# Kernel tuning notes

Measured on AMD Instinct MI355X. Metric: run time of the kernel, lower is better.

The kernel has to match this reference:

```python
import jax, jax.numpy as jnp
import numpy as np

B = 262144
INPUT_DIM = 512
HID = 64
NUM_BASE = 2
NUM_CLASSES = 2


def setup_inputs() -> dict:
    key = jax.random.key(0)
    ks = jax.random.split(key, 10)
    probs = jax.random.uniform(ks[0], (B, NUM_BASE, NUM_CLASSES), dtype=jnp.float32)
    fuzzy_features = jax.random.normal(ks[1], (B, INPUT_DIM), dtype=jnp.float32)
    s1 = 1.0 / np.sqrt(INPUT_DIM)
    s2 = 1.0 / np.sqrt(HID)
    # m1: Linear(input_dim,64) -> ReLU -> Linear(64, num_base*num_classes)
    W1 = jax.random.uniform(ks[2], (INPUT_DIM, HID), jnp.float32, -s1, s1)
    b1 = jax.random.uniform(ks[3], (HID,), jnp.float32, -s1, s1)
    W2 = jax.random.uniform(ks[4], (HID, NUM_BASE * NUM_CLASSES), jnp.float32, -s2, s2)
    b2 = jax.random.uniform(ks[5], (NUM_BASE * NUM_CLASSES,), jnp.float32, -s2, s2)
    # m2: Linear(input_dim,64) -> ReLU -> Linear(64, num_classes)
    W3 = jax.random.uniform(ks[6], (INPUT_DIM, HID), jnp.float32, -s1, s1)
    b3 = jax.random.uniform(ks[7], (HID,), jnp.float32, -s1, s1)
    W4 = jax.random.uniform(ks[8], (HID, NUM_CLASSES), jnp.float32, -s2, s2)
    b4 = jax.random.uniform(ks[9], (NUM_CLASSES,), jnp.float32, -s2, s2)
    return {"probs": probs, "fuzzy_features": fuzzy_features,
            "W1": W1, "b1": b1, "W2": W2, "b2": b2,
            "W3": W3, "b3": b3, "W4": W4, "b4": b4}


def _forward(probs, x, W1, b1, W2, b2, W3, b3, W4, b4):
    # FuzzyMeasureLearner
    h1 = jax.nn.relu(x @ W1 + b1)                       # [B, 64]
    single = jax.nn.sigmoid((h1 @ W2 + b2).reshape(-1, NUM_BASE, NUM_CLASSES))
    h2 = jax.nn.relu(x @ W3 + b3)                       # [B, 64]
    inc = jax.nn.sigmoid(h2 @ W4 + b4)                  # [B, 2]
    # Vectorized Choquet integral (binary, 2 sources)
    p0 = probs[:, 0, :]                                 # [B, 2]
    p1 = probs[:, 1, :]
    mu1 = single[:, 0, :]
    mu2 = single[:, 1, :]
    mu12 = jnp.minimum(jnp.maximum(mu1, mu2) + inc, 1.0)
    res = jnp.where(p0 <= p1,
                    p0 * mu1 + (p1 - p0) * mu12,
                    p1 * mu2 + (p0 - p1) * mu12)        # [B, 2]
    return jax.nn.softmax(res, axis=1)


def reference(probs, fuzzy_features, W1, b1, W2, b2, W3, b3, W4, b4):
    return _forward(probs, fuzzy_features, W1, b1, W2, b2, W3, b3, W4, b4)
```

## Files before the change

### kernel.cpp

```cpp
#include <hip/hip_runtime.h>

typedef short s16x8 __attribute__((ext_vector_type(8)));
typedef float f32x4 __attribute__((ext_vector_type(4)));
typedef float f32x2 __attribute__((ext_vector_type(2)));

static __device__ __forceinline__ short f2bf(float f) {
    unsigned u = __builtin_bit_cast(unsigned, f);
    unsigned r = (u + 0x7fffu + ((u >> 16) & 1u)) >> 16;
    return (short)r;
}

__global__ void prep_weights(const float* __restrict__ W1,
                             const float* __restrict__ W3,
                             short* __restrict__ bws) {
    int tid = blockIdx.x * blockDim.x + threadIdx.x;
    int j  = tid & 7;
    int l  = (tid >> 3) & 63;
    int nt = (tid >> 9) & 7;
    int kk = tid >> 12;
    int k = kk * 32 + ((l >> 4) << 3) + j;
    int n = nt * 16 + (l & 15);
    float v = (n < 64) ? W1[k * 64 + n] : W3[k * 64 + (n - 64)];
    bws[tid] = f2bf(v);
}

__global__ __launch_bounds__(256, 2)
void mf2_main(const float* __restrict__ probs, const float* __restrict__ x,
              const short* __restrict__ bws,
              const float* __restrict__ b1, const float* __restrict__ W2,
              const float* __restrict__ b2, const float* __restrict__ b3,
              const float* __restrict__ W4, const float* __restrict__ b4,
              float* __restrict__ out)
{
    const int lane = threadIdx.x & 63;
    const int wv   = threadIdx.x >> 6;
    const int g    = lane >> 4;
    const int m    = lane & 15;
    const long rowBase = (long)blockIdx.x * 128 + wv * 32;

    float w2r[4][4];
    float w4r[4][2];
    float biasr[8];
    #pragma unroll
    for (int nt = 0; nt < 4; ++nt) {
        const int col = m + 16 * nt;
        #pragma unroll
        for (int c = 0; c < 4; ++c) w2r[nt][c] = W2[col * 4 + c];
        #pragma unroll
        for (int c = 0; c < 2; ++c) w4r[nt][c] = W4[col * 2 + c];
    }
    #pragma unroll
    for (int nt = 0; nt < 8; ++nt) {
        const int col = m + 16 * nt;
        biasr[nt] = (col < 64) ? b1[col] : b3[col - 64];
    }
    float b2v[4], b4v[2];
    #pragma unroll
    for (int c = 0; c < 4; ++c) b2v[c] = b2[c];
    #pragma unroll
    for (int c = 0; c < 2; ++c) b4v[c] = b4[c];

    f32x4 acc[2][8];
    #pragma unroll
    for (int t = 0; t < 2; ++t)
        #pragma unroll
        for (int nt = 0; nt < 8; ++nt)
            acc[t][nt] = (f32x4){0.f, 0.f, 0.f, 0.f};

    const float* xp = x + (rowBase + m) * 512 + g * 8;

    #pragma unroll 2
    for (int kk = 0; kk < 16; ++kk) {
        s16x8 a[2];
        #pragma unroll
        for (int t = 0; t < 2; ++t) {
            const float* p = xp + t * (16 * 512) + kk * 32;
            f32x4 lo = *(const f32x4*)p;
            f32x4 hi = *(const f32x4*)(p + 4);
            s16x8 av;
            av[0] = f2bf(lo[0]); av[1] = f2bf(lo[1]);
            av[2] = f2bf(lo[2]); av[3] = f2bf(lo[3]);
            av[4] = f2bf(hi[0]); av[5] = f2bf(hi[1]);
            av[6] = f2bf(hi[2]); av[7] = f2bf(hi[3]);
            a[t] = av;
        }
        const s16x8* bp = (const s16x8*)(bws + kk * 4096) + lane;
        #pragma unroll
        for (int nt = 0; nt < 8; ++nt) {
            s16x8 b = bp[nt * 64];
            acc[0][nt] = __builtin_amdgcn_mfma_f32_16x16x32_bf16(a[0], b, acc[0][nt], 0, 0, 0);
            acc[1][nt] = __builtin_amdgcn_mfma_f32_16x16x32_bf16(a[1], b, acc[1][nt], 0, 0, 0);
        }
    }

    float own[6] = {0.f, 0.f, 0.f, 0.f, 0.f, 0.f};
    #pragma unroll
    for (int t = 0; t < 2; ++t) {
        #pragma unroll
        for (int r = 0; r < 4; ++r) {
            float v[6] = {0.f, 0.f, 0.f, 0.f, 0.f, 0.f};
            #pragma unroll
            for (int nt = 0; nt < 4; ++nt) {
                float h = fmaxf(acc[t][nt][r] + biasr[nt], 0.f);
                v[0] += h * w2r[nt][0];
                v[1] += h * w2r[nt][1];
                v[2] += h * w2r[nt][2];
                v[3] += h * w2r[nt][3];
            }
            #pragma unroll
            for (int j = 0; j < 4; ++j) {
                float h = fmaxf(acc[t][4 + j][r] + biasr[4 + j], 0.f);
                v[4] += h * w4r[j][0];
                v[5] += h * w4r[j][1];
            }
            #pragma unroll
            for (int msk = 1; msk <= 8; msk <<= 1) {
                #pragma unroll
                for (int c = 0; c < 6; ++c) v[c] += __shfl_xor(v[c], msk, 64);
            }
            if (m == t * 4 + r) {
                #pragma unroll
                for (int c = 0; c < 6; ++c) own[c] = v[c];
            }
        }
    }

    if (m < 8) {
        const int t = m >> 2, r = m & 3;
        const long row = rowBase + t * 16 + g * 4 + r;
        f32x4 pr = *(const f32x4*)(probs + row * 4);
        float mu1[2], mu2[2], icv[2];
        #pragma unroll
        for (int c = 0; c < 2; ++c) {
            mu1[c] = 1.0f / (1.0f + __expf(-(own[c]     + b2v[c])));
            mu2[c] = 1.0f / (1.0f + __expf(-(own[2 + c] + b2v[2 + c])));
            icv[c] = 1.0f / (1.0f + __expf(-(own[4 + c] + b4v[c])));
        }
        float res[2];
        #pragma unroll
        for (int c = 0; c < 2; ++c) {
            float p0 = pr[c], p1 = pr[2 + c];
            float m12 = fminf(fmaxf(mu1[c], mu2[c]) + icv[c], 1.0f);
            res[c] = (p0 <= p1) ? (p0 * mu1[c] + (p1 - p0) * m12)
                                : (p1 * mu2[c] + (p0 - p1) * m12);
        }
        float d01 = res[0] - res[1];
        f32x2 o;
        o[0] = 1.0f / (1.0f + __expf(-d01));
        o[1] = 1.0f / (1.0f + __expf(d01));
        *(f32x2*)(out + row * 2) = o;
    }
}

extern "C" void kernel_launch(void* const* d_in, const int* in_sizes, int n_in,
                              void* d_out, int out_size, void* d_ws, size_t ws_size,
                              hipStream_t stream)
{
    const float* probs = (const float*)d_in[0];
    const float* x     = (const float*)d_in[1];
    const float* W1    = (const float*)d_in[2];
    const float* b1    = (const float*)d_in[3];
    const float* W2    = (const float*)d_in[4];
    const float* b2    = (const float*)d_in[5];
    const float* W3    = (const float*)d_in[6];
    const float* b3    = (const float*)d_in[7];
    const float* W4    = (const float*)d_in[8];
    const float* b4    = (const float*)d_in[9];
    float* out = (float*)d_out;
    short* bws = (short*)d_ws;

    hipLaunchKernelGGL(prep_weights, dim3(256), dim3(256), 0, stream, W1, W3, bws);
    hipLaunchKernelGGL(mf2_main, dim3(2048), dim3(256), 0, stream,
                       probs, x, bws, b1, W2, b2, b3, W4, b4, out);
}
```

Before: 143.4 us.

## Double rows per wave, prefetch x one K-step ahead, packed bf16 convert

Each wave now handles 64 rows instead of 32, so each B-weight fragment load is reused across four M tiles, and the grid is halved. The x loads for the next K step are issued before the MFMAs of the current step, as nontemporal loads, to overlap global latency with compute. Float-to-bf16 conversion uses the packed intrinsic instead of manual rounding, and the W2/W4 loads are vectorised. Accumulator registers double (128 VGPRs of accumulators), which may strain the 2-waves-per-SIMD launch bound and cause spills or lower occupancy.

```diff
diff --git a/kernel.cpp b/kernel.cpp
--- a/kernel.cpp
+++ b/kernel.cpp
@@ -1,6 +1,8 @@
 #include <hip/hip_runtime.h>
+#include <hip/hip_bf16.h>
 
 typedef short s16x8 __attribute__((ext_vector_type(8)));
+typedef unsigned u32x4 __attribute__((ext_vector_type(4)));
 typedef float f32x4 __attribute__((ext_vector_type(4)));
 typedef float f32x2 __attribute__((ext_vector_type(2)));
 
@@ -8,6 +10,13 @@
     unsigned u = __builtin_bit_cast(unsigned, f);
     unsigned r = (u + 0x7fffu + ((u >> 16) & 1u)) >> 16;
     return (short)r;
+}
+
+static __device__ __forceinline__ unsigned pk2bf(float a, float b) {
+    __hip_bfloat162 h = __float22bfloat162_rn(make_float2(a, b));
+    unsigned r;
+    __builtin_memcpy(&r, &h, sizeof(r));
+    return r;
 }
 
 __global__ void prep_weights(const float* __restrict__ W1,
@@ -36,7 +45,58 @@
     const int wv   = threadIdx.x >> 6;
     const int g    = lane >> 4;
     const int m    = lane & 15;
-    const long rowBase = (long)blockIdx.x * 128 + wv * 32;
+    const long rowBase = (long)blockIdx.x * 256 + wv * 64;
+
+    f32x4 acc[4][8];
+    #pragma unroll
+    for (int t = 0; t < 4; ++t)
+        #pragma unroll
+        for (int nt = 0; nt < 8; ++nt)
+            acc[t][nt] = (f32x4){0.f, 0.f, 0.f, 0.f};
+
+    const float* xp = x + (rowBase + m) * 512 + g * 8;
+    const s16x8* bp = (const s16x8*)bws + lane;
+
+    f32x4 ra[4][2];
+    #pragma unroll
+    for (int t = 0; t < 4; ++t) {
+        const float* p = xp + t * (16 * 512);
+        ra[t][0] = __builtin_nontemporal_load((const f32x4*)p);
+        ra[t][1] = __builtin_nontemporal_load((const f32x4*)(p + 4));
+    }
+
+    #pragma unroll 2
+    for (int kk = 0; kk < 16; ++kk) {
+        s16x8 b[8];
+        #pragma unroll
+        for (int nt = 0; nt < 8; ++nt) b[nt] = bp[kk * 512 + nt * 64];
+
+        s16x8 a[4];
+        #pragma unroll
+        for (int t = 0; t < 4; ++t) {
+            u32x4 pa;
+            pa[0] = pk2bf(ra[t][0][0], ra[t][0][1]);
+            pa[1] = pk2bf(ra[t][0][2], ra[t][0][3]);
+            pa[2] = pk2bf(ra[t][1][0], ra[t][1][1]);
+            pa[3] = pk2bf(ra[t][1][2], ra[t][1][3]);
+            a[t] = __builtin_bit_cast(s16x8, pa);
+        }
+
+        if (kk < 15) {
+            #pragma unroll
+            for (int t = 0; t < 4; ++t) {
+                const float* p = xp + t * (16 * 512) + (kk + 1) * 32;
+                ra[t][0] = __builtin_nontemporal_load((const f32x4*)p);
+                ra[t][1] = __builtin_nontemporal_load((const f32x4*)(p + 4));
+            }
+        }
+
+        #pragma unroll
+        for (int nt = 0; nt < 8; ++nt)
+            #pragma unroll
+            for (int t = 0; t < 4; ++t)
+                acc[t][nt] = __builtin_amdgcn_mfma_f32_16x16x32_bf16(a[t], b[nt], acc[t][nt], 0, 0, 0);
+    }
 
     float w2r[4][4];
     float w4r[4][2];
@@ -44,10 +104,11 @@
     #pragma unroll
     for (int nt = 0; nt < 4; ++nt) {
         const int col = m + 16 * nt;
-        #pragma unroll
-        for (int c = 0; c < 4; ++c) w2r[nt][c] = W2[col * 4 + c];
-        #pragma unroll
-        for (int c = 0; c < 2; ++c) w4r[nt][c] = W4[col * 2 + c];
+        f32x4 w2v = *(const f32x4*)(W2 + col * 4);
+        #pragma unroll
+        for (int c = 0; c < 4; ++c) w2r[nt][c] = w2v[c];
+        f32x2 w4v = *(const f32x2*)(W4 + col * 2);
+        w4r[nt][0] = w4v[0]; w4r[nt][1] = w4v[1];
     }
     #pragma unroll
     for (int nt = 0; nt < 8; ++nt) {
@@ -60,42 +121,9 @@
     #pragma unroll
     for (int c = 0; c < 2; ++c) b4v[c] = b4[c];
 
-    f32x4 acc[2][8];
-    #pragma unroll
-    for (int t = 0; t < 2; ++t)
-        #pragma unroll
-        for (int nt = 0; nt < 8; ++nt)
-            acc[t][nt] = (f32x4){0.f, 0.f, 0.f, 0.f};
-
-    const float* xp = x + (rowBase + m) * 512 + g * 8;
-
-    #pragma unroll 2
-    for (int kk = 0; kk < 16; ++kk) {
-        s16x8 a[2];
-        #pragma unroll
-        for (int t = 0; t < 2; ++t) {
-            const float* p = xp + t * (16 * 512) + kk * 32;
-            f32x4 lo = *(const f32x4*)p;
-            f32x4 hi = *(const f32x4*)(p + 4);
-            s16x8 av;
-            av[0] = f2bf(lo[0]); av[1] = f2bf(lo[1]);
-            av[2] = f2bf(lo[2]); av[3] = f2bf(lo[3]);
-            av[4] = f2bf(hi[0]); av[5] = f2bf(hi[1]);
-            av[6] = f2bf(hi[2]); av[7] = f2bf(hi[3]);
-            a[t] = av;
-        }
-        const s16x8* bp = (const s16x8*)(bws + kk * 4096) + lane;
-        #pragma unroll
-        for (int nt = 0; nt < 8; ++nt) {
-            s16x8 b = bp[nt * 64];
-            acc[0][nt] = __builtin_amdgcn_mfma_f32_16x16x32_bf16(a[0], b, acc[0][nt], 0, 0, 0);
-            acc[1][nt] = __builtin_amdgcn_mfma_f32_16x16x32_bf16(a[1], b, acc[1][nt], 0, 0, 0);
-        }
-    }
-
     float own[6] = {0.f, 0.f, 0.f, 0.f, 0.f, 0.f};
     #pragma unroll
-    for (int t = 0; t < 2; ++t) {
+    for (int t = 0; t < 4; ++t) {
         #pragma unroll
         for (int r = 0; r < 4; ++r) {
             float v[6] = {0.f, 0.f, 0.f, 0.f, 0.f, 0.f};
@@ -125,7 +153,7 @@
         }
     }
 
-    if (m < 8) {
+    {
         const int t = m >> 2, r = m & 3;
         const long row = rowBase + t * 16 + g * 4 + r;
         f32x4 pr = *(const f32x4*)(probs + row * 4);
@@ -170,6 +198,6 @@
     short* bws = (short*)d_ws;
 
     hipLaunchKernelGGL(prep_weights, dim3(256), dim3(256), 0, stream, W1, W3, bws);
-    hipLaunchKernelGGL(mf2_main, dim3(2048), dim3(256), 0, stream,
+    hipLaunchKernelGGL(mf2_main, dim3(1024), dim3(256), 0, stream,
                        probs, x, bws, b1, W2, b2, b3, W4, b4, out);
 }
```

New measurement: 146.4 us. +2.1%, slower.

## Stage bf16 weights in LDS with 1024-thread blocks and packed bf16 conversion

Applied to the files above, without the earlier changes.

Each block now copies the whole 128 KB pre-packed bf16 weight matrix into shared memory and reads B fragments from LDS instead of global memory. Blocks grow to 1024 threads covering 512 rows, and the grid shrinks to 512. The fp32-to-bf16 conversion of x switches to the packed two-element HIP intrinsic, and loads of the epilogue weights and biases move after the MFMA loop to lower register pressure during it. The cost is a 128 KB LDS footprint per block, which likely limits occupancy to one block per CU, and a copy-in phase plus barrier before any compute.

```diff
diff --git a/kernel.cpp b/kernel.cpp
--- a/kernel.cpp
+++ b/kernel.cpp
@@ -1,6 +1,8 @@
 #include <hip/hip_runtime.h>
+#include <hip/hip_bf16.h>
 
 typedef short s16x8 __attribute__((ext_vector_type(8)));
+typedef unsigned u32x4 __attribute__((ext_vector_type(4)));
 typedef float f32x4 __attribute__((ext_vector_type(4)));
 typedef float f32x2 __attribute__((ext_vector_type(2)));
 
@@ -8,6 +10,13 @@
     unsigned u = __builtin_bit_cast(unsigned, f);
     unsigned r = (u + 0x7fffu + ((u >> 16) & 1u)) >> 16;
     return (short)r;
+}
+
+static __device__ __forceinline__ unsigned pk2bf(float a, float b) {
+    __hip_bfloat162 h = __float22bfloat162_rn(make_float2(a, b));
+    unsigned r;
+    __builtin_memcpy(&r, &h, sizeof(r));
+    return r;
 }
 
 __global__ void prep_weights(const float* __restrict__ W1,
@@ -24,7 +33,7 @@
     bws[tid] = f2bf(v);
 }
 
-__global__ __launch_bounds__(256, 2)
+__global__ __launch_bounds__(1024, 4)
 void mf2_main(const float* __restrict__ probs, const float* __restrict__ x,
               const short* __restrict__ bws,
               const float* __restrict__ b1, const float* __restrict__ W2,
@@ -32,11 +41,58 @@
               const float* __restrict__ W4, const float* __restrict__ b4,
               float* __restrict__ out)
 {
-    const int lane = threadIdx.x & 63;
-    const int wv   = threadIdx.x >> 6;
+    __shared__ short bsh[512 * 128];
+
+    const int tid  = threadIdx.x;
+    const int lane = tid & 63;
+    const int wv   = tid >> 6;
     const int g    = lane >> 4;
     const int m    = lane & 15;
-    const long rowBase = (long)blockIdx.x * 128 + wv * 32;
+    const long rowBase = (long)blockIdx.x * 512 + wv * 32;
+
+    {
+        const f32x4* src = (const f32x4*)bws;
+        f32x4* dst = (f32x4*)bsh;
+        #pragma unroll
+        for (int it = 0; it < 8; ++it) {
+            const int idx = it * 1024 + tid;
+            dst[idx] = src[idx];
+        }
+    }
+    __syncthreads();
+
+    f32x4 acc[2][8];
+    #pragma unroll
+    for (int t = 0; t < 2; ++t)
+        #pragma unroll
+        for (int nt = 0; nt < 8; ++nt)
+            acc[t][nt] = (f32x4){0.f, 0.f, 0.f, 0.f};
+
+    const float* xp = x + (rowBase + m) * 512 + g * 8;
+    const s16x8* bls = (const s16x8*)bsh + lane;
+
+    #pragma unroll 2
+    for (int kk = 0; kk < 16; ++kk) {
+        s16x8 a[2];
+        #pragma unroll
+        for (int t = 0; t < 2; ++t) {
+            const float* p = xp + t * (16 * 512) + kk * 32;
+            f32x4 lo = *(const f32x4*)p;
+            f32x4 hi = *(const f32x4*)(p + 4);
+            u32x4 pa;
+            pa[0] = pk2bf(lo[0], lo[1]);
+            pa[1] = pk2bf(lo[2], lo[3]);
+            pa[2] = pk2bf(hi[0], hi[1]);
+            pa[3] = pk2bf(hi[2], hi[3]);
+            a[t] = __builtin_bit_cast(s16x8, pa);
+        }
+        #pragma unroll
+        for (int nt = 0; nt < 8; ++nt) {
+            s16x8 b = bls[kk * 512 + nt * 64];
+            acc[0][nt] = __builtin_amdgcn_mfma_f32_16x16x32_bf16(a[0], b, acc[0][nt], 0, 0, 0);
+            acc[1][nt] = __builtin_amdgcn_mfma_f32_16x16x32_bf16(a[1], b, acc[1][nt], 0, 0, 0);
+        }
+    }
 
     float w2r[4][4];
     float w4r[4][2];
@@ -44,10 +100,11 @@
     #pragma unroll
     for (int nt = 0; nt < 4; ++nt) {
         const int col = m + 16 * nt;
+        f32x4 w2v = *(const f32x4*)(W2 + col * 4);
         #pragma unroll
-        for (int c = 0; c < 4; ++c) w2r[nt][c] = W2[col * 4 + c];
-        #pragma unroll
-        for (int c = 0; c < 2; ++c) w4r[nt][c] = W4[col * 2 + c];
+        for (int c = 0; c < 4; ++c) w2r[nt][c] = w2v[c];
+        f32x2 w4v = *(const f32x2*)(W4 + col * 2);
+        w4r[nt][0] = w4v[0]; w4r[nt][1] = w4v[1];
     }
     #pragma unroll
     for (int nt = 0; nt < 8; ++nt) {
@@ -59,39 +116,6 @@
     for (int c = 0; c < 4; ++c) b2v[c] = b2[c];
     #pragma unroll
     for (int c = 0; c < 2; ++c) b4v[c] = b4[c];
-
-    f32x4 acc[2][8];
-    #pragma unroll
-    for (int t = 0; t < 2; ++t)
-        #pragma unroll
-        for (int nt = 0; nt < 8; ++nt)
-            acc[t][nt] = (f32x4){0.f, 0.f, 0.f, 0.f};
-
-    const float* xp = x + (rowBase + m) * 512 + g * 8;
-
-    #pragma unroll 2
-    for (int kk = 0; kk < 16; ++kk) {
-        s16x8 a[2];
-        #pragma unroll
-        for (int t = 0; t < 2; ++t) {
-            const float* p = xp + t * (16 * 512) + kk * 32;
-            f32x4 lo = *(const f32x4*)p;
-            f32x4 hi = *(const f32x4*)(p + 4);
-            s16x8 av;
-            av[0] = f2bf(lo[0]); av[1] = f2bf(lo[1]);
-            av[2] = f2bf(lo[2]); av[3] = f2bf(lo[3]);
-            av[4] = f2bf(hi[0]); av[5] = f2bf(hi[1]);
-            av[6] = f2bf(hi[2]); av[7] = f2bf(hi[3]);
-            a[t] = av;
-        }
-        const s16x8* bp = (const s16x8*)(bws + kk * 4096) + lane;
-        #pragma unroll
-        for (int nt = 0; nt < 8; ++nt) {
-            s16x8 b = bp[nt * 64];
-            acc[0][nt] = __builtin_amdgcn_mfma_f32_16x16x32_bf16(a[0], b, acc[0][nt], 0, 0, 0);
-            acc[1][nt] = __builtin_amdgcn_mfma_f32_16x16x32_bf16(a[1], b, acc[1][nt], 0, 0, 0);
-        }
-    }
 
     float own[6] = {0.f, 0.f, 0.f, 0.f, 0.f, 0.f};
     #pragma unroll
@@ -170,6 +194,6 @@
     short* bws = (short*)d_ws;
 
     hipLaunchKernelGGL(prep_weights, dim3(256), dim3(256), 0, stream, W1, W3, bws);
-    hipLaunchKernelGGL(mf2_main, dim3(2048), dim3(256), 0, stream,
+    hipLaunchKernelGGL(mf2_main, dim3(512), dim3(1024), 0, stream,
                        probs, x, bws, b1, W2, b2, b3, W4, b4, out);
 }
```

Result: faster. 125.9 us (-12.2%).
